# Kernel optimization log

Hardware: AMD Instinct MI355X
Metric: run time of the kernel (lower is better)

## Reference

```python
import jax, jax.numpy as jnp
import numpy as np

B = 2048        # batch of plans
N_LEAF = 1024   # scan nodes (leaves of complete binary tree)
F = 32          # node feature dim
H = 128         # neural-unit hidden dim
O = 32          # unit output dim = 1 (latency) + data_vec_dim (31)


def _mlp_params(key, in_dim, scale=0.05):
    k1, k2, k3 = jax.random.split(key, 3)
    return (
        jax.random.normal(k1, (in_dim, H), jnp.float32) * scale, jnp.zeros((H,), jnp.float32),
        jax.random.normal(k2, (H, H), jnp.float32) * scale, jnp.zeros((H,), jnp.float32),
        jax.random.normal(k3, (H, O), jnp.float32) * scale, jnp.zeros((O,), jnp.float32),
    )


def setup_inputs() -> dict:
    key = jax.random.key(0)
    k1, k2, k3, k4 = jax.random.split(key, 4)
    leaf_feats = jax.random.normal(k1, (B, N_LEAF, F), jnp.float32)
    # internal nodes stored level-by-level bottom-up: 512, 256, ..., 1  (total 1023)
    internal_feats = jax.random.normal(k2, (B, N_LEAF - 1, F), jnp.float32)
    sW1, sb1, sW2, sb2, sW3, sb3 = _mlp_params(k3, F)           # Scan unit (0 children)
    jW1, jb1, jW2, jb2, jW3, jb3 = _mlp_params(k4, F + 2 * O)   # Join unit (2 children)
    return dict(leaf_feats=leaf_feats, internal_feats=internal_feats,
                sW1=sW1, sb1=sb1, sW2=sW2, sb2=sb2, sW3=sW3, sb3=sb3,
                jW1=jW1, jb1=jb1, jW2=jW2, jb2=jb2, jW3=jW3, jb3=jb3)


def _unit(x, W1, b1, W2, b2, W3, b3):
    # Neural unit: 2 hidden ReLU layers -> O outputs (latency + data vector)
    h = jax.nn.relu(x @ W1 + b1)
    h = jax.nn.relu(h @ W2 + b2)
    return h @ W3 + b3


def reference(leaf_feats, internal_feats,
              sW1, sb1, sW2, sb2, sW3, sb3,
              jW1, jb1, jW2, jb2, jW3, jb3):
    # Leaves: Scan unit on node features alone
    cur = _unit(leaf_feats, sW1, sb1, sW2, sb2, sW3, sb3)  # [B, 1024, O]
    off, n = 0, N_LEAF // 2
    while n >= 1:  # static loop over tree levels (bottom-up)
        feats = internal_feats[:, off:off + n]             # [B, n, F]
        children = cur.reshape(B, n, 2 * O)                # concat of 2 child outputs
        x = jnp.concatenate([feats, children], axis=-1)    # [B, n, F + 2O]
        cur = _unit(x, jW1, jb1, jW2, jb2, jW3, jb3)       # [B, n, O]
        off += n
        n //= 2
    return cur[:, 0, 0]  # root latency (output[:, 0]) per plan -> [B]
```

## Files before the change

kernel.cpp:

```cpp
#include <hip/hip_runtime.h>
#include <hip/hip_bf16.h>


typedef _Float16 f16;
typedef _Float16 f16x8 __attribute__((ext_vector_type(8)));
typedef _Float16 f16x4 __attribute__((ext_vector_type(4)));
typedef float    f32x4 __attribute__((ext_vector_type(4)));

#define MFMA16(a, b, c) __builtin_amdgcn_mfma_f32_16x16x32_f16((a), (b), (c), 0, 0, 0)

#define OFF_S1 0
#define OFF_S2 4096
#define OFF_S3 20480
#define OFF_J1 24576
#define OFF_J2 36864
#define OFF_J3 53248
#define W_TOTAL 57344
#define CURA_BYTE_OFF 114688

__global__ void prep_weights(const float* __restrict__ sW1,
                             const float* __restrict__ sW2,
                             const float* __restrict__ sW3,
                             const float* __restrict__ jW1,
                             const float* __restrict__ jW2,
                             const float* __restrict__ jW3,
                             f16* __restrict__ wbuf)
{
    int idx = blockIdx.x * 256 + threadIdx.x;
    if (idx >= W_TOTAL) return;
    const float* W;
    int off, M, K;
    if (idx < OFF_S2)      { off = OFF_S1; M = 128; K = 32;  W = sW1; }
    else if (idx < OFF_S3) { off = OFF_S2; M = 128; K = 128; W = sW2; }
    else if (idx < OFF_J1) { off = OFF_S3; M = 32;  K = 128; W = sW3; }
    else if (idx < OFF_J2) { off = OFF_J1; M = 128; K = 96;  W = jW1; }
    else if (idx < OFF_J3) { off = OFF_J2; M = 128; K = 128; W = jW2; }
    else                   { off = OFF_J3; M = 32;  K = 128; W = jW3; }
    int r = idx - off;
    int m = r / K;
    int k = r - m * K;
    wbuf[idx] = (f16)W[(size_t)k * M + m];
}

__device__ __forceinline__ void gload16(const void* g, void* l)
{
    __builtin_amdgcn_global_load_lds(
        (const __attribute__((address_space(1))) void*)g,
        (__attribute__((address_space(3))) void*)l,
        16, 0, 0);
}

template <bool LEAF>
__global__ __launch_bounds__(256, 3)
void mlp_level(const float* __restrict__ feats,
               const f16*   __restrict__ cur_in,
               f16*         __restrict__ cur_out,
               float*       __restrict__ out_final,
               const f16*   __restrict__ W1t,
               const f16*   __restrict__ W2t,
               const f16*   __restrict__ W3t,
               const float* __restrict__ b1,
               const float* __restrict__ b2,
               const float* __restrict__ b3,
               int rows, int log2n, int foff, int is_last)
{
    constexpr int K1    = LEAF ? 32 : 96;
    constexpr int NK1   = LEAF ? 1 : 3;
    constexpr int PITCH = 136;

    __shared__ __align__(16) f16   h1[32 * PITCH];
    __shared__ __align__(16) f16   h2[32 * PITCH];
    __shared__ __align__(16) float fstage[2][32 * 32];
    __shared__ __align__(16) f16   cstage[(LEAF ? 1 : 2)][32 * 64];

    const int tid  = threadIdx.x;
    const int wave = tid >> 6;
    const int lane = tid & 63;
    const int n    = lane & 15;
    const int q    = lane >> 4;
    const int n7   = n & 7;
    const int mrow = 32 * wave;
    const int l3g  = wave & 1;
    const int l3h  = wave >> 1;

    const int srow   = (wave << 3) + (lane >> 3);
    const int schunk = (lane & 7) ^ (lane >> 3);

    f16x8 A1[2][NK1], A2[2][4], A3[4];
#pragma unroll
    for (int mt = 0; mt < 2; ++mt)
#pragma unroll
        for (int ks = 0; ks < NK1; ++ks)
            A1[mt][ks] = *(const f16x8*)(W1t + (size_t)(mrow + 16 * mt + n) * K1 + 32 * ks + 8 * q);
#pragma unroll
    for (int mt = 0; mt < 2; ++mt)
#pragma unroll
        for (int ks = 0; ks < 4; ++ks)
            A2[mt][ks] = *(const f16x8*)(W2t + (size_t)(mrow + 16 * mt + n) * 128 + 32 * ks + 8 * q);
#pragma unroll
    for (int ks = 0; ks < 4; ++ks)
        A3[ks] = *(const f16x8*)(W3t + (size_t)(16 * l3h + n) * 128 + 32 * ks + 8 * q);

    f32x4 bf1[2], bf2[2], bf3;
#pragma unroll
    for (int mt = 0; mt < 2; ++mt) {
        bf1[mt] = *(const f32x4*)(b1 + mrow + 16 * mt + 4 * q);
        bf2[mt] = *(const f32x4*)(b2 + mrow + 16 * mt + 4 * q);
    }
    bf3 = *(const f32x4*)(b3 + 16 * l3h + 4 * q);

    auto stage = [&](int tg0, int sb) {
        int gr = tg0 + srow;
        const float* fsrc;
        if constexpr (LEAF) {
            fsrc = feats + (size_t)gr * 32 + schunk * 4;
        } else {
            int bb = gr >> log2n;
            int ii = gr & ((1 << log2n) - 1);
            fsrc = feats + ((size_t)bb * 1023 + foff + ii) * 32 + schunk * 4;
        }
        gload16(fsrc, &fstage[sb][wave * 256]);
        if constexpr (!LEAF)
            gload16(cur_in + (size_t)gr * 64 + schunk * 8, &cstage[sb][wave * 512]);
    };

    const int stride = gridDim.x * 32;
    int g0 = blockIdx.x * 32;
    if (g0 >= rows) return;

    int rb = 0;
    stage(g0, 0);

    for (; g0 < rows; g0 += stride) {
        int gnext = g0 + stride;
        stage(gnext < rows ? gnext : g0, rb ^ 1);

        if constexpr (LEAF) asm volatile("s_waitcnt vmcnt(1)" ::: "memory");
        else                asm volatile("s_waitcnt vmcnt(2)" ::: "memory");
        __builtin_amdgcn_s_barrier();

        f32x4 C[2][2];
#pragma unroll
        for (int g = 0; g < 2; ++g)
#pragma unroll
            for (int mt = 0; mt < 2; ++mt) C[g][mt] = bf1[mt];

#pragma unroll
        for (int g = 0; g < 2; ++g) {
            const int r = 16 * g + n;
            f32x4 fa = *(const f32x4*)(&fstage[rb][r * 32 + (((2 * q)     ^ n7) * 4)]);
            f32x4 fb = *(const f32x4*)(&fstage[rb][r * 32 + (((2 * q + 1) ^ n7) * 4)]);
            f16x8 Bf;
#pragma unroll
            for (int j = 0; j < 4; ++j) {
                Bf[j]     = (f16)fa[j];
                Bf[4 + j] = (f16)fb[j];
            }
#pragma unroll
            for (int mt = 0; mt < 2; ++mt) C[g][mt] = MFMA16(A1[mt][0], Bf, C[g][mt]);
            if constexpr (!LEAF) {
                f16x8 cl = *(const f16x8*)(&cstage[rb][r * 64 + ((q       ^ n7) * 8)]);
                f16x8 cr = *(const f16x8*)(&cstage[rb][r * 64 + (((4 + q) ^ n7) * 8)]);
#pragma unroll
                for (int mt = 0; mt < 2; ++mt) C[g][mt] = MFMA16(A1[mt][1], cl, C[g][mt]);
#pragma unroll
                for (int mt = 0; mt < 2; ++mt) C[g][mt] = MFMA16(A1[mt][2], cr, C[g][mt]);
            }
        }
#pragma unroll
        for (int g = 0; g < 2; ++g)
#pragma unroll
            for (int mt = 0; mt < 2; ++mt) {
                f16x4 pk;
                pk[0] = (f16)fmaxf(C[g][mt][0], 0.0f);
                pk[1] = (f16)fmaxf(C[g][mt][1], 0.0f);
                pk[2] = (f16)fmaxf(C[g][mt][2], 0.0f);
                pk[3] = (f16)fmaxf(C[g][mt][3], 0.0f);
                *(f16x4*)(h1 + (16 * g + n) * PITCH + mrow + 16 * mt + 4 * q) = pk;
            }
        asm volatile("s_waitcnt lgkmcnt(0)" ::: "memory");
        __builtin_amdgcn_s_barrier();

#pragma unroll
        for (int g = 0; g < 2; ++g)
#pragma unroll
            for (int mt = 0; mt < 2; ++mt) C[g][mt] = bf2[mt];
#pragma unroll
        for (int ks = 0; ks < 4; ++ks)
#pragma unroll
            for (int g = 0; g < 2; ++g) {
                f16x8 Bf = *(const f16x8*)(h1 + (16 * g + n) * PITCH + 32 * ks + 8 * q);
#pragma unroll
                for (int mt = 0; mt < 2; ++mt) C[g][mt] = MFMA16(A2[mt][ks], Bf, C[g][mt]);
            }
#pragma unroll
        for (int g = 0; g < 2; ++g)
#pragma unroll
            for (int mt = 0; mt < 2; ++mt) {
                f16x4 pk;
                pk[0] = (f16)fmaxf(C[g][mt][0], 0.0f);
                pk[1] = (f16)fmaxf(C[g][mt][1], 0.0f);
                pk[2] = (f16)fmaxf(C[g][mt][2], 0.0f);
                pk[3] = (f16)fmaxf(C[g][mt][3], 0.0f);
                *(f16x4*)(h2 + (16 * g + n) * PITCH + mrow + 16 * mt + 4 * q) = pk;
            }
        asm volatile("s_waitcnt lgkmcnt(0)" ::: "memory");
        __builtin_amdgcn_s_barrier();

        f32x4 C3 = bf3;
#pragma unroll
        for (int ks = 0; ks < 4; ++ks) {
            f16x8 Bf = *(const f16x8*)(h2 + (16 * l3g + n) * PITCH + 32 * ks + 8 * q);
            C3 = MFMA16(A3[ks], Bf, C3);
        }

        if (is_last) {
            if (l3h == 0 && q == 0) out_final[g0 + 16 * l3g + n] = C3[0];
        } else {
            f16x4 pk;
            pk[0] = (f16)C3[0]; pk[1] = (f16)C3[1]; pk[2] = (f16)C3[2]; pk[3] = (f16)C3[3];
            *(f16x4*)(cur_out + (size_t)(g0 + 16 * l3g + n) * 32 + 16 * l3h + 4 * q) = pk;
        }

        rb ^= 1;
    }
}

extern "C" void kernel_launch(void* const* d_in, const int* in_sizes, int n_in,
                              void* d_out, int out_size, void* d_ws, size_t ws_size,
                              hipStream_t stream)
{
    const float* leaf_feats     = (const float*)d_in[0];
    const float* internal_feats = (const float*)d_in[1];
    const float* sW1 = (const float*)d_in[2];  const float* sb1 = (const float*)d_in[3];
    const float* sW2 = (const float*)d_in[4];  const float* sb2 = (const float*)d_in[5];
    const float* sW3 = (const float*)d_in[6];  const float* sb3 = (const float*)d_in[7];
    const float* jW1 = (const float*)d_in[8];  const float* jb1 = (const float*)d_in[9];
    const float* jW2 = (const float*)d_in[10]; const float* jb2 = (const float*)d_in[11];
    const float* jW3 = (const float*)d_in[12]; const float* jb3 = (const float*)d_in[13];

    f16* wbuf = (f16*)d_ws;
    f16* curA = (f16*)((char*)d_ws + CURA_BYTE_OFF);
    f16* curB = (f16*)((char*)d_ws + CURA_BYTE_OFF + 134217728);

    prep_weights<<<(W_TOTAL + 255) / 256, 256, 0, stream>>>(
        sW1, sW2, sW3, jW1, jW2, jW3, wbuf);

    mlp_level<true><<<2048, 256, 0, stream>>>(
        leaf_feats, nullptr, curA, nullptr,
        wbuf + OFF_S1, wbuf + OFF_S2, wbuf + OFF_S3,
        sb1, sb2, sb3,
        2048 * 1024, 0, 0, 0);

    const f16* cin = curA;
    f16* cout = curB;
    int off = 0, lg = 9;
    for (int nlev = 512; nlev >= 1; nlev >>= 1, --lg) {
        int rows  = 2048 * nlev;
        int iters = rows / 32;
        int grid  = iters < 2048 ? iters : 2048;
        mlp_level<false><<<grid, 256, 0, stream>>>(
            internal_feats, cin, cout, (float*)d_out,
            wbuf + OFF_J1, wbuf + OFF_J2, wbuf + OFF_J3,
            jb1, jb2, jb3,
            rows, lg, off, (nlev == 1) ? 1 : 0);
        off += nlev;
        f16* t = cout; cout = (f16*)cin; cin = t;
    }
}
```

Baseline: 787.5 us.

## Software-pipeline the three MLP layers across tiles with one barrier per stage

```diff
diff --git a/kernel.cpp b/kernel.cpp
--- a/kernel.cpp
+++ b/kernel.cpp
@@ -8,6 +8,10 @@
 typedef float    f32x4 __attribute__((ext_vector_type(4)));
 
 #define MFMA16(a, b, c) __builtin_amdgcn_mfma_f32_16x16x32_f16((a), (b), (c), 0, 0, 0)
+
+#define VMCNT(N) asm volatile("s_waitcnt vmcnt(" #N ")" ::: "memory")
+#define LGKM0    asm volatile("s_waitcnt lgkmcnt(0)" ::: "memory")
+#define BARRIER() do { __builtin_amdgcn_s_barrier(); __builtin_amdgcn_sched_barrier(0); } while (0)
 
 #define OFF_S1 0
 #define OFF_S2 4096
@@ -50,7 +54,7 @@
         16, 0, 0);
 }
 
-template <bool LEAF>
+template <bool LEAF, bool LAST>
 __global__ __launch_bounds__(256, 3)
 void mlp_level(const float* __restrict__ feats,
                const f16*   __restrict__ cur_in,
@@ -62,16 +66,16 @@
                const float* __restrict__ b1,
                const float* __restrict__ b2,
                const float* __restrict__ b3,
-               int rows, int log2n, int foff, int is_last)
+               int log2n, int foff, int nt)
 {
-    constexpr int K1    = LEAF ? 32 : 96;
-    constexpr int NK1   = LEAF ? 1 : 3;
-    constexpr int PITCH = 136;
-
-    __shared__ __align__(16) f16   h1[32 * PITCH];
-    __shared__ __align__(16) f16   h2[32 * PITCH];
-    __shared__ __align__(16) float fstage[2][32 * 32];
+    constexpr int K1  = LEAF ? 32 : 96;
+    constexpr int NK1 = LEAF ? 1 : 3;
+
+    __shared__ __align__(16) f16   h1[2][32 * 128];
+    __shared__ __align__(16) f16   h2[2][32 * 128];
+    __shared__ __align__(16) float fstage[3][32 * 32];
     __shared__ __align__(16) f16   cstage[(LEAF ? 1 : 2)][32 * 64];
+    __shared__ __align__(16) float bias_lds[288];
 
     const int tid  = threadIdx.x;
     const int wave = tid >> 6;
@@ -86,6 +90,10 @@
     const int srow   = (wave << 3) + (lane >> 3);
     const int schunk = (lane & 7) ^ (lane >> 3);
 
+    if (tid < 128) bias_lds[tid] = b1[tid];
+    else           bias_lds[tid] = b2[tid - 128];
+    if (tid < 32)  bias_lds[256 + tid] = b3[tid];
+
     f16x8 A1[2][NK1], A2[2][4], A3[4];
 #pragma unroll
     for (int mt = 0; mt < 2; ++mt)
@@ -101,15 +109,10 @@
     for (int ks = 0; ks < 4; ++ks)
         A3[ks] = *(const f16x8*)(W3t + (size_t)(16 * l3h + n) * 128 + 32 * ks + 8 * q);
 
-    f32x4 bf1[2], bf2[2], bf3;
-#pragma unroll
-    for (int mt = 0; mt < 2; ++mt) {
-        bf1[mt] = *(const f32x4*)(b1 + mrow + 16 * mt + 4 * q);
-        bf2[mt] = *(const f32x4*)(b2 + mrow + 16 * mt + 4 * q);
-    }
-    bf3 = *(const f32x4*)(b3 + 16 * l3h + 4 * q);
-
-    auto stage = [&](int tg0, int sb) {
+    const int stride = gridDim.x * 32;
+    const int base   = blockIdx.x * 32;
+
+    auto stage_f = [&](int tg0, int sb) {
         int gr = tg0 + srow;
         const float* fsrc;
         if constexpr (LEAF) {
@@ -120,47 +123,35 @@
             fsrc = feats + ((size_t)bb * 1023 + foff + ii) * 32 + schunk * 4;
         }
         gload16(fsrc, &fstage[sb][wave * 256]);
-        if constexpr (!LEAF)
-            gload16(cur_in + (size_t)gr * 64 + schunk * 8, &cstage[sb][wave * 512]);
-    };
-
-    const int stride = gridDim.x * 32;
-    int g0 = blockIdx.x * 32;
-    if (g0 >= rows) return;
-
-    int rb = 0;
-    stage(g0, 0);
-
-    for (; g0 < rows; g0 += stride) {
-        int gnext = g0 + stride;
-        stage(gnext < rows ? gnext : g0, rb ^ 1);
-
-        if constexpr (LEAF) asm volatile("s_waitcnt vmcnt(1)" ::: "memory");
-        else                asm volatile("s_waitcnt vmcnt(2)" ::: "memory");
-        __builtin_amdgcn_s_barrier();
-
+    };
+    auto stage_c = [&](int tg0, int sb) {
+        int gr = tg0 + srow;
+        gload16(cur_in + (size_t)gr * 64 + schunk * 8, &cstage[sb][wave * 512]);
+    };
+
+    auto doL1 = [&](int t, int g0) {
+        const int fb = t % 3;
+        const int hb = t & 1;
         f32x4 C[2][2];
 #pragma unroll
-        for (int g = 0; g < 2; ++g)
-#pragma unroll
-            for (int mt = 0; mt < 2; ++mt) C[g][mt] = bf1[mt];
-
+        for (int mt = 0; mt < 2; ++mt) {
+            f32x4 bv = *(const f32x4*)&bias_lds[mrow + 16 * mt + 4 * q];
+            C[0][mt] = bv; C[1][mt] = bv;
+        }
 #pragma unroll
         for (int g = 0; g < 2; ++g) {
             const int r = 16 * g + n;
-            f32x4 fa = *(const f32x4*)(&fstage[rb][r * 32 + (((2 * q)     ^ n7) * 4)]);
-            f32x4 fb = *(const f32x4*)(&fstage[rb][r * 32 + (((2 * q + 1) ^ n7) * 4)]);
+            f32x4 fa = *(const f32x4*)&fstage[fb][r * 32 + (((2 * q)     ^ n7) << 2)];
+            f32x4 fv = *(const f32x4*)&fstage[fb][r * 32 + (((2 * q + 1) ^ n7) << 2)];
             f16x8 Bf;
 #pragma unroll
-            for (int j = 0; j < 4; ++j) {
-                Bf[j]     = (f16)fa[j];
-                Bf[4 + j] = (f16)fb[j];
-            }
+            for (int j = 0; j < 4; ++j) { Bf[j] = (f16)fa[j]; Bf[4 + j] = (f16)fv[j]; }
 #pragma unroll
             for (int mt = 0; mt < 2; ++mt) C[g][mt] = MFMA16(A1[mt][0], Bf, C[g][mt]);
             if constexpr (!LEAF) {
-                f16x8 cl = *(const f16x8*)(&cstage[rb][r * 64 + ((q       ^ n7) * 8)]);
-                f16x8 cr = *(const f16x8*)(&cstage[rb][r * 64 + (((4 + q) ^ n7) * 8)]);
+                const int cb = t & 1;
+                f16x8 cl = *(const f16x8*)&cstage[cb][r * 64 + (( q      ^ n7) << 3)];
+                f16x8 cr = *(const f16x8*)&cstage[cb][r * 64 + (((4 + q) ^ n7) << 3)];
 #pragma unroll
                 for (int mt = 0; mt < 2; ++mt) C[g][mt] = MFMA16(A1[mt][1], cl, C[g][mt]);
 #pragma unroll
@@ -176,20 +167,24 @@
                 pk[1] = (f16)fmaxf(C[g][mt][1], 0.0f);
                 pk[2] = (f16)fmaxf(C[g][mt][2], 0.0f);
                 pk[3] = (f16)fmaxf(C[g][mt][3], 0.0f);
-                *(f16x4*)(h1 + (16 * g + n) * PITCH + mrow + 16 * mt + 4 * q) = pk;
+                const int ch = 4 * wave + 2 * mt + (q >> 1);
+                *(f16x4*)&h1[hb][(16 * g + n) * 128 + ((ch ^ n7) << 3) + 4 * (q & 1)] = pk;
             }
-        asm volatile("s_waitcnt lgkmcnt(0)" ::: "memory");
-        __builtin_amdgcn_s_barrier();
-
-#pragma unroll
-        for (int g = 0; g < 2; ++g)
-#pragma unroll
-            for (int mt = 0; mt < 2; ++mt) C[g][mt] = bf2[mt];
+    };
+
+    auto doL2 = [&](int t) {
+        const int hb = t & 1;
+        f32x4 C[2][2];
+#pragma unroll
+        for (int mt = 0; mt < 2; ++mt) {
+            f32x4 bv = *(const f32x4*)&bias_lds[128 + mrow + 16 * mt + 4 * q];
+            C[0][mt] = bv; C[1][mt] = bv;
+        }
 #pragma unroll
         for (int ks = 0; ks < 4; ++ks)
 #pragma unroll
             for (int g = 0; g < 2; ++g) {
-                f16x8 Bf = *(const f16x8*)(h1 + (16 * g + n) * PITCH + 32 * ks + 8 * q);
+                f16x8 Bf = *(const f16x8*)&h1[hb][(16 * g + n) * 128 + (((4 * ks + q) ^ n7) << 3)];
 #pragma unroll
                 for (int mt = 0; mt < 2; ++mt) C[g][mt] = MFMA16(A2[mt][ks], Bf, C[g][mt]);
             }
@@ -202,27 +197,87 @@
                 pk[1] = (f16)fmaxf(C[g][mt][1], 0.0f);
                 pk[2] = (f16)fmaxf(C[g][mt][2], 0.0f);
                 pk[3] = (f16)fmaxf(C[g][mt][3], 0.0f);
-                *(f16x4*)(h2 + (16 * g + n) * PITCH + mrow + 16 * mt + 4 * q) = pk;
+                const int ch = 4 * wave + 2 * mt + (q >> 1);
+                *(f16x4*)&h2[hb][(16 * g + n) * 128 + ((ch ^ n7) << 3) + 4 * (q & 1)] = pk;
             }
-        asm volatile("s_waitcnt lgkmcnt(0)" ::: "memory");
-        __builtin_amdgcn_s_barrier();
-
-        f32x4 C3 = bf3;
+    };
+
+    auto doL3 = [&](int t, int g0) {
+        const int hb = t & 1;
+        f32x4 C3 = *(const f32x4*)&bias_lds[256 + 16 * l3h + 4 * q];
 #pragma unroll
         for (int ks = 0; ks < 4; ++ks) {
-            f16x8 Bf = *(const f16x8*)(h2 + (16 * l3g + n) * PITCH + 32 * ks + 8 * q);
+            f16x8 Bf = *(const f16x8*)&h2[hb][(16 * l3g + n) * 128 + (((4 * ks + q) ^ n7) << 3)];
             C3 = MFMA16(A3[ks], Bf, C3);
         }
-
-        if (is_last) {
+        if constexpr (LAST) {
             if (l3h == 0 && q == 0) out_final[g0 + 16 * l3g + n] = C3[0];
         } else {
             f16x4 pk;
             pk[0] = (f16)C3[0]; pk[1] = (f16)C3[1]; pk[2] = (f16)C3[2]; pk[3] = (f16)C3[3];
             *(f16x4*)(cur_out + (size_t)(g0 + 16 * l3g + n) * 32 + 16 * l3h + 4 * q) = pk;
         }
-
-        rb ^= 1;
+    };
+
+    stage_f(base, 0);
+    if (nt > 1) stage_f(base + stride, 1);
+    if constexpr (!LEAF) stage_c(base, 0);
+    LGKM0;
+
+    if (nt >= 6) {
+        if constexpr (LEAF) { VMCNT(1); } else { VMCNT(0); }
+        BARRIER();
+        if constexpr (!LEAF) stage_c(base + stride, 1);
+        stage_f(base + 2 * stride, 2);
+        doL1(0, base);
+        LGKM0;
+        VMCNT(1); BARRIER();
+        if constexpr (!LEAF) stage_c(base + 2 * stride, 0);
+        stage_f(base + 3 * stride, 0);
+        doL1(1, base + stride); doL2(0);
+        LGKM0;
+        VMCNT(1); BARRIER();
+        if constexpr (!LEAF) stage_c(base + 3 * stride, 1);
+        stage_f(base + 4 * stride, 1);
+        doL1(2, base + 2 * stride); doL2(1); doL3(0, base);
+        LGKM0;
+        VMCNT(2); BARRIER();
+        if constexpr (!LEAF) stage_c(base + 4 * stride, 0);
+        stage_f(base + 5 * stride, 2);
+        doL1(3, base + 3 * stride); doL2(2); doL3(1, base + stride);
+        LGKM0;
+        for (int p = 4; p <= nt - 2; ++p) {
+            if constexpr (LEAF) { VMCNT(3); } else { VMCNT(2); }
+            BARRIER();
+            if constexpr (!LEAF) stage_c(base + (p + 1) * stride, (p + 1) & 1);
+            if (p + 2 < nt) stage_f(base + (p + 2) * stride, (p + 2) % 3);
+            doL1(p, base + p * stride);
+            doL2(p - 1);
+            doL3(p - 2, base + (p - 2) * stride);
+            LGKM0;
+        }
+        if constexpr (LEAF) { VMCNT(2); } else { VMCNT(1); }
+        BARRIER();
+        doL1(nt - 1, base + (nt - 1) * stride);
+        doL2(nt - 2);
+        doL3(nt - 3, base + (nt - 3) * stride);
+        LGKM0;
+        BARRIER();
+        doL2(nt - 1);
+        doL3(nt - 2, base + (nt - 2) * stride);
+        LGKM0;
+        BARRIER();
+        doL3(nt - 1, base + (nt - 1) * stride);
+    } else {
+        for (int p = 0; p <= nt + 1; ++p) {
+            VMCNT(0); BARRIER();
+            if constexpr (!LEAF) { if (p + 1 < nt) stage_c(base + (p + 1) * stride, (p + 1) & 1); }
+            if (p + 2 < nt) stage_f(base + (p + 2) * stride, (p + 2) % 3);
+            if (p < nt)              doL1(p, base + p * stride);
+            if (p >= 1 && p <= nt)   doL2(p - 1);
+            if (p >= 2)              doL3(p - 2, base + (p - 2) * stride);
+            LGKM0;
+        }
     }
 }
 
@@ -246,11 +301,11 @@
     prep_weights<<<(W_TOTAL + 255) / 256, 256, 0, stream>>>(
         sW1, sW2, sW3, jW1, jW2, jW3, wbuf);
 
-    mlp_level<true><<<2048, 256, 0, stream>>>(
+    mlp_level<true, false><<<2048, 256, 0, stream>>>(
         leaf_feats, nullptr, curA, nullptr,
         wbuf + OFF_S1, wbuf + OFF_S2, wbuf + OFF_S3,
         sb1, sb2, sb3,
-        2048 * 1024, 0, 0, 0);
+        0, 0, 32);
 
     const f16* cin = curA;
     f16* cout = curB;
@@ -259,11 +314,20 @@
         int rows  = 2048 * nlev;
         int iters = rows / 32;
         int grid  = iters < 2048 ? iters : 2048;
-        mlp_level<false><<<grid, 256, 0, stream>>>(
-            internal_feats, cin, cout, (float*)d_out,
-            wbuf + OFF_J1, wbuf + OFF_J2, wbuf + OFF_J3,
-            jb1, jb2, jb3,
-            rows, lg, off, (nlev == 1) ? 1 : 0);
+        int nt    = iters / grid;
+        if (nlev == 1) {
+            mlp_level<false, true><<<grid, 256, 0, stream>>>(
+                internal_feats, cin, cout, (float*)d_out,
+                wbuf + OFF_J1, wbuf + OFF_J2, wbuf + OFF_J3,
+                jb1, jb2, jb3,
+                lg, off, nt);
+        } else {
+            mlp_level<false, false><<<grid, 256, 0, stream>>>(
+                internal_feats, cin, cout, (float*)d_out,
+                wbuf + OFF_J1, wbuf + OFF_J2, wbuf + OFF_J3,
+                jb1, jb2, jb3,
+                lg, off, nt);
+        }
         off += nlev;
         f16* t = cout; cout = (f16*)cin; cin = t;
     }
```

Result: slower. 856.4 us (+8.7%).

## Software-pipeline MLP levels with register prefetch and fuse top tree levels into one tail kernel

Applied to the files above, without the earlier changes.

```diff
diff --git a/kernel.cpp b/kernel.cpp
--- a/kernel.cpp
+++ b/kernel.cpp
@@ -1,5 +1,4 @@
 #include <hip/hip_runtime.h>
-#include <hip/hip_bf16.h>
 
 
 typedef _Float16 f16;
@@ -8,6 +7,8 @@
 typedef float    f32x4 __attribute__((ext_vector_type(4)));
 
 #define MFMA16(a, b, c) __builtin_amdgcn_mfma_f32_16x16x32_f16((a), (b), (c), 0, 0, 0)
+#define LGKM0    asm volatile("s_waitcnt lgkmcnt(0)" ::: "memory")
+#define BARRIER() do { __builtin_amdgcn_s_barrier(); __builtin_amdgcn_sched_barrier(0); } while (0)
 
 #define OFF_S1 0
 #define OFF_S2 4096
@@ -42,36 +43,25 @@
     wbuf[idx] = (f16)W[(size_t)k * M + m];
 }
 
-__device__ __forceinline__ void gload16(const void* g, void* l)
-{
-    __builtin_amdgcn_global_load_lds(
-        (const __attribute__((address_space(1))) void*)g,
-        (__attribute__((address_space(3))) void*)l,
-        16, 0, 0);
-}
-
 template <bool LEAF>
-__global__ __launch_bounds__(256, 3)
+__global__ __launch_bounds__(256, LEAF ? 4 : 3)
 void mlp_level(const float* __restrict__ feats,
                const f16*   __restrict__ cur_in,
                f16*         __restrict__ cur_out,
-               float*       __restrict__ out_final,
                const f16*   __restrict__ W1t,
                const f16*   __restrict__ W2t,
                const f16*   __restrict__ W3t,
                const float* __restrict__ b1,
                const float* __restrict__ b2,
                const float* __restrict__ b3,
-               int rows, int log2n, int foff, int is_last)
+               int log2n, int foff, int nt)
 {
-    constexpr int K1    = LEAF ? 32 : 96;
-    constexpr int NK1   = LEAF ? 1 : 3;
-    constexpr int PITCH = 136;
-
-    __shared__ __align__(16) f16   h1[32 * PITCH];
-    __shared__ __align__(16) f16   h2[32 * PITCH];
-    __shared__ __align__(16) float fstage[2][32 * 32];
-    __shared__ __align__(16) f16   cstage[(LEAF ? 1 : 2)][32 * 64];
+    constexpr int K1  = LEAF ? 32 : 96;
+    constexpr int NK1 = LEAF ? 1 : 3;
+
+    __shared__ __align__(16) f16   h1[32 * 128];
+    __shared__ __align__(16) f16   h2[2][32 * 128];
+    __shared__ __align__(16) float bias_lds[288];
 
     const int tid  = threadIdx.x;
     const int wave = tid >> 6;
@@ -83,8 +73,9 @@
     const int l3g  = wave & 1;
     const int l3h  = wave >> 1;
 
-    const int srow   = (wave << 3) + (lane >> 3);
-    const int schunk = (lane & 7) ^ (lane >> 3);
+    if (tid < 128) bias_lds[tid] = b1[tid];
+    else           bias_lds[tid] = b2[tid - 128];
+    if (tid < 32)  bias_lds[256 + tid] = b3[tid];
 
     f16x8 A1[2][NK1], A2[2][4], A3[4];
 #pragma unroll
@@ -101,70 +92,49 @@
     for (int ks = 0; ks < 4; ++ks)
         A3[ks] = *(const f16x8*)(W3t + (size_t)(16 * l3h + n) * 128 + 32 * ks + 8 * q);
 
-    f32x4 bf1[2], bf2[2], bf3;
-#pragma unroll
-    for (int mt = 0; mt < 2; ++mt) {
-        bf1[mt] = *(const f32x4*)(b1 + mrow + 16 * mt + 4 * q);
-        bf2[mt] = *(const f32x4*)(b2 + mrow + 16 * mt + 4 * q);
-    }
-    bf3 = *(const f32x4*)(b3 + 16 * l3h + 4 * q);
-
-    auto stage = [&](int tg0, int sb) {
-        int gr = tg0 + srow;
-        const float* fsrc;
-        if constexpr (LEAF) {
-            fsrc = feats + (size_t)gr * 32 + schunk * 4;
-        } else {
-            int bb = gr >> log2n;
-            int ii = gr & ((1 << log2n) - 1);
-            fsrc = feats + ((size_t)bb * 1023 + foff + ii) * 32 + schunk * 4;
-        }
-        gload16(fsrc, &fstage[sb][wave * 256]);
-        if constexpr (!LEAF)
-            gload16(cur_in + (size_t)gr * 64 + schunk * 8, &cstage[sb][wave * 512]);
+    LGKM0; BARRIER();
+
+    struct PF { f32x4 fa[2], fb[2]; f16x8 cl[2], cr[2]; };
+    auto load_pf = [&](int g0, PF& p) {
+#pragma unroll
+        for (int g = 0; g < 2; ++g) {
+            int gr = g0 + 16 * g + n;
+            const float* frow;
+            if constexpr (LEAF) {
+                frow = feats + (size_t)gr * 32;
+            } else {
+                int bb = gr >> log2n;
+                int ii = gr & ((1 << log2n) - 1);
+                frow = feats + ((size_t)bb * 1023 + foff + ii) * 32;
+            }
+            p.fa[g] = *(const f32x4*)(frow + 8 * q);
+            p.fb[g] = *(const f32x4*)(frow + 8 * q + 4);
+            if constexpr (!LEAF) {
+                p.cl[g] = *(const f16x8*)(cur_in + (size_t)(2 * gr) * 32 + 8 * q);
+                p.cr[g] = *(const f16x8*)(cur_in + (size_t)(2 * gr) * 32 + 32 + 8 * q);
+            }
+        }
     };
 
-    const int stride = gridDim.x * 32;
-    int g0 = blockIdx.x * 32;
-    if (g0 >= rows) return;
-
-    int rb = 0;
-    stage(g0, 0);
-
-    for (; g0 < rows; g0 += stride) {
-        int gnext = g0 + stride;
-        stage(gnext < rows ? gnext : g0, rb ^ 1);
-
-        if constexpr (LEAF) asm volatile("s_waitcnt vmcnt(1)" ::: "memory");
-        else                asm volatile("s_waitcnt vmcnt(2)" ::: "memory");
-        __builtin_amdgcn_s_barrier();
-
+    auto doL1 = [&](const PF& p) {
         f32x4 C[2][2];
 #pragma unroll
-        for (int g = 0; g < 2; ++g)
-#pragma unroll
-            for (int mt = 0; mt < 2; ++mt) C[g][mt] = bf1[mt];
-
+        for (int mt = 0; mt < 2; ++mt) {
+            f32x4 bv = *(const f32x4*)&bias_lds[mrow + 16 * mt + 4 * q];
+            C[0][mt] = bv; C[1][mt] = bv;
+        }
 #pragma unroll
         for (int g = 0; g < 2; ++g) {
-            const int r = 16 * g + n;
-            f32x4 fa = *(const f32x4*)(&fstage[rb][r * 32 + (((2 * q)     ^ n7) * 4)]);
-            f32x4 fb = *(const f32x4*)(&fstage[rb][r * 32 + (((2 * q + 1) ^ n7) * 4)]);
             f16x8 Bf;
 #pragma unroll
-            for (int j = 0; j < 4; ++j) {
-                Bf[j]     = (f16)fa[j];
-                Bf[4 + j] = (f16)fb[j];
-            }
+            for (int j = 0; j < 4; ++j) { Bf[j] = (f16)p.fa[g][j]; Bf[4 + j] = (f16)p.fb[g][j]; }
 #pragma unroll
             for (int mt = 0; mt < 2; ++mt) C[g][mt] = MFMA16(A1[mt][0], Bf, C[g][mt]);
             if constexpr (!LEAF) {
-                f16x8 cl = *(const f16x8*)(&cstage[rb][r * 64 + ((q       ^ n7) * 8)]);
-                f16x8 cr = *(const f16x8*)(&cstage[rb][r * 64 + (((4 + q) ^ n7) * 8)]);
-#pragma unroll
-                for (int mt = 0; mt < 2; ++mt) C[g][mt] = MFMA16(A1[mt][1], cl, C[g][mt]);
-#pragma unroll
-                for (int mt = 0; mt < 2; ++mt) C[g][mt] = MFMA16(A1[mt][2], cr, C[g][mt]);
+#pragma unroll
+                for (int mt = 0; mt < 2; ++mt) C[g][mt] = MFMA16(A1[mt][1], p.cl[g], C[g][mt]);
+#pragma unroll
+                for (int mt = 0; mt < 2; ++mt) C[g][mt] = MFMA16(A1[mt][2], p.cr[g], C[g][mt]);
             }
         }
 #pragma unroll
@@ -176,23 +146,29 @@
                 pk[1] = (f16)fmaxf(C[g][mt][1], 0.0f);
                 pk[2] = (f16)fmaxf(C[g][mt][2], 0.0f);
                 pk[3] = (f16)fmaxf(C[g][mt][3], 0.0f);
-                *(f16x4*)(h1 + (16 * g + n) * PITCH + mrow + 16 * mt + 4 * q) = pk;
-            }
-        asm volatile("s_waitcnt lgkmcnt(0)" ::: "memory");
-        __builtin_amdgcn_s_barrier();
-
-#pragma unroll
-        for (int g = 0; g < 2; ++g)
-#pragma unroll
-            for (int mt = 0; mt < 2; ++mt) C[g][mt] = bf2[mt];
+                const int ch = 4 * wave + 2 * mt + (q >> 1);
+                *(f16x4*)&h1[(16 * g + n) * 128 + ((ch ^ n7) << 3) + 4 * (q & 1)] = pk;
+            }
+    };
+
+    auto doL2 = [&](int t) {
+        const int hb = t & 1;
+        f32x4 C[2][2];
+#pragma unroll
+        for (int mt = 0; mt < 2; ++mt) {
+            f32x4 bv = *(const f32x4*)&bias_lds[128 + mrow + 16 * mt + 4 * q];
+            C[0][mt] = bv; C[1][mt] = bv;
+        }
+        __builtin_amdgcn_s_setprio(1);
 #pragma unroll
         for (int ks = 0; ks < 4; ++ks)
 #pragma unroll
             for (int g = 0; g < 2; ++g) {
-                f16x8 Bf = *(const f16x8*)(h1 + (16 * g + n) * PITCH + 32 * ks + 8 * q);
+                f16x8 Bf = *(const f16x8*)&h1[(16 * g + n) * 128 + (((4 * ks + q) ^ n7) << 3)];
 #pragma unroll
                 for (int mt = 0; mt < 2; ++mt) C[g][mt] = MFMA16(A2[mt][ks], Bf, C[g][mt]);
             }
+        __builtin_amdgcn_s_setprio(0);
 #pragma unroll
         for (int g = 0; g < 2; ++g)
 #pragma unroll
@@ -202,27 +178,199 @@
                 pk[1] = (f16)fmaxf(C[g][mt][1], 0.0f);
                 pk[2] = (f16)fmaxf(C[g][mt][2], 0.0f);
                 pk[3] = (f16)fmaxf(C[g][mt][3], 0.0f);
-                *(f16x4*)(h2 + (16 * g + n) * PITCH + mrow + 16 * mt + 4 * q) = pk;
-            }
-        asm volatile("s_waitcnt lgkmcnt(0)" ::: "memory");
-        __builtin_amdgcn_s_barrier();
-
-        f32x4 C3 = bf3;
+                const int ch = 4 * wave + 2 * mt + (q >> 1);
+                *(f16x4*)&h2[hb][(16 * g + n) * 128 + ((ch ^ n7) << 3) + 4 * (q & 1)] = pk;
+            }
+    };
+
+    auto doL3 = [&](int t, int g0) {
+        const int hb = t & 1;
+        f32x4 C3 = *(const f32x4*)&bias_lds[256 + 16 * l3h + 4 * q];
 #pragma unroll
         for (int ks = 0; ks < 4; ++ks) {
-            f16x8 Bf = *(const f16x8*)(h2 + (16 * l3g + n) * PITCH + 32 * ks + 8 * q);
+            f16x8 Bf = *(const f16x8*)&h2[hb][(16 * l3g + n) * 128 + (((4 * ks + q) ^ n7) << 3)];
             C3 = MFMA16(A3[ks], Bf, C3);
         }
-
-        if (is_last) {
-            if (l3h == 0 && q == 0) out_final[g0 + 16 * l3g + n] = C3[0];
-        } else {
-            f16x4 pk;
-            pk[0] = (f16)C3[0]; pk[1] = (f16)C3[1]; pk[2] = (f16)C3[2]; pk[3] = (f16)C3[3];
-            *(f16x4*)(cur_out + (size_t)(g0 + 16 * l3g + n) * 32 + 16 * l3h + 4 * q) = pk;
-        }
-
-        rb ^= 1;
+        f16x4 pk;
+        pk[0] = (f16)C3[0]; pk[1] = (f16)C3[1]; pk[2] = (f16)C3[2]; pk[3] = (f16)C3[3];
+        *(f16x4*)(cur_out + (size_t)(g0 + 16 * l3g + n) * 32 + 16 * l3h + 4 * q) = pk;
+    };
+
+    const int stride = gridDim.x * 32;
+    const int base   = blockIdx.x * 32;
+
+    PF p;
+    load_pf(base, p);
+    for (int t = 0; t < nt; ++t) {
+        const int g0 = base + t * stride;
+        PF pn;
+        if (t + 1 < nt) load_pf(g0 + stride, pn);
+        doL1(p);
+        if (t > 0) doL3(t - 1, g0 - stride);
+        LGKM0; BARRIER();
+        doL2(t);
+        LGKM0; BARRIER();
+        if (t + 1 < nt) p = pn;
+    }
+    doL3(nt - 1, base + (nt - 1) * stride);
+}
+
+__global__ __launch_bounds__(256, 2)
+void mlp_tail(const float* __restrict__ feats,
+              const f16*   __restrict__ cur_in,
+              float*       __restrict__ out_final,
+              const f16*   __restrict__ W1t,
+              const f16*   __restrict__ W2t,
+              const f16*   __restrict__ W3t,
+              const float* __restrict__ b1,
+              const float* __restrict__ b2,
+              const float* __restrict__ b3)
+{
+    __shared__ __align__(16) f16   h1[32 * 128];
+    __shared__ __align__(16) f16   h2[32 * 128];
+    __shared__ __align__(16) f16   cur_lds[32 * 32];
+    __shared__ __align__(16) float bias_lds[288];
+
+    const int tid  = threadIdx.x;
+    const int wave = tid >> 6;
+    const int lane = tid & 63;
+    const int n    = lane & 15;
+    const int q    = lane >> 4;
+    const int n7   = n & 7;
+    const int mrow = 32 * wave;
+    const int l3g  = wave & 1;
+    const int l3h  = wave >> 1;
+    const int b0   = blockIdx.x * 2;
+
+    if (tid < 128) bias_lds[tid] = b1[tid];
+    else           bias_lds[tid] = b2[tid - 128];
+    if (tid < 32)  bias_lds[256 + tid] = b3[tid];
+
+    f16x8 A1[2][3], A2[2][4], A3[4];
+#pragma unroll
+    for (int mt = 0; mt < 2; ++mt)
+#pragma unroll
+        for (int ks = 0; ks < 3; ++ks)
+            A1[mt][ks] = *(const f16x8*)(W1t + (size_t)(mrow + 16 * mt + n) * 96 + 32 * ks + 8 * q);
+#pragma unroll
+    for (int mt = 0; mt < 2; ++mt)
+#pragma unroll
+        for (int ks = 0; ks < 4; ++ks)
+            A2[mt][ks] = *(const f16x8*)(W2t + (size_t)(mrow + 16 * mt + n) * 128 + 32 * ks + 8 * q);
+#pragma unroll
+    for (int ks = 0; ks < 4; ++ks)
+        A3[ks] = *(const f16x8*)(W3t + (size_t)(16 * l3h + n) * 128 + 32 * ks + 8 * q);
+
+    LGKM0; BARRIER();
+
+    int nlev = 16, lg = 4, fo = 992;
+    for (int lev = 0; lev < 5; ++lev) {
+        const int rows_t = 2 * nlev;
+        f32x4 fa[2], fb[2];
+        f16x8 cl[2], cr[2];
+#pragma unroll
+        for (int g = 0; g < 2; ++g) {
+            int r   = 16 * g + n;
+            int sel = (r >> lg) & 1;
+            int i   = r & (nlev - 1);
+            int rc  = sel * nlev + i;
+            const float* frow = feats + ((size_t)(b0 + sel) * 1023 + fo + i) * 32;
+            fa[g] = *(const f32x4*)(frow + 8 * q);
+            fb[g] = *(const f32x4*)(frow + 8 * q + 4);
+            if (lev == 0) {
+                int gr = (b0 + sel) * 16 + i;
+                cl[g] = *(const f16x8*)(cur_in + (size_t)(2 * gr) * 32 + 8 * q);
+                cr[g] = *(const f16x8*)(cur_in + (size_t)(2 * gr) * 32 + 32 + 8 * q);
+            } else {
+                cl[g] = *(const f16x8*)&cur_lds[(2 * rc) * 32 + 8 * q];
+                cr[g] = *(const f16x8*)&cur_lds[(2 * rc) * 32 + 32 + 8 * q];
+            }
+        }
+        {
+            f32x4 C[2][2];
+#pragma unroll
+            for (int mt = 0; mt < 2; ++mt) {
+                f32x4 bv = *(const f32x4*)&bias_lds[mrow + 16 * mt + 4 * q];
+                C[0][mt] = bv; C[1][mt] = bv;
+            }
+#pragma unroll
+            for (int g = 0; g < 2; ++g) {
+                f16x8 Bf;
+#pragma unroll
+                for (int j = 0; j < 4; ++j) { Bf[j] = (f16)fa[g][j]; Bf[4 + j] = (f16)fb[g][j]; }
+#pragma unroll
+                for (int mt = 0; mt < 2; ++mt) C[g][mt] = MFMA16(A1[mt][0], Bf, C[g][mt]);
+#pragma unroll
+                for (int mt = 0; mt < 2; ++mt) C[g][mt] = MFMA16(A1[mt][1], cl[g], C[g][mt]);
+#pragma unroll
+                for (int mt = 0; mt < 2; ++mt) C[g][mt] = MFMA16(A1[mt][2], cr[g], C[g][mt]);
+            }
+#pragma unroll
+            for (int g = 0; g < 2; ++g)
+#pragma unroll
+                for (int mt = 0; mt < 2; ++mt) {
+                    f16x4 pk;
+                    pk[0] = (f16)fmaxf(C[g][mt][0], 0.0f);
+                    pk[1] = (f16)fmaxf(C[g][mt][1], 0.0f);
+                    pk[2] = (f16)fmaxf(C[g][mt][2], 0.0f);
+                    pk[3] = (f16)fmaxf(C[g][mt][3], 0.0f);
+                    const int ch = 4 * wave + 2 * mt + (q >> 1);
+                    *(f16x4*)&h1[(16 * g + n) * 128 + ((ch ^ n7) << 3) + 4 * (q & 1)] = pk;
+                }
+        }
+        LGKM0; BARRIER();
+        {
+            f32x4 C[2][2];
+#pragma unroll
+            for (int mt = 0; mt < 2; ++mt) {
+                f32x4 bv = *(const f32x4*)&bias_lds[128 + mrow + 16 * mt + 4 * q];
+                C[0][mt] = bv; C[1][mt] = bv;
+            }
+#pragma unroll
+            for (int ks = 0; ks < 4; ++ks)
+#pragma unroll
+                for (int g = 0; g < 2; ++g) {
+                    f16x8 Bf = *(const f16x8*)&h1[(16 * g + n) * 128 + (((4 * ks + q) ^ n7) << 3)];
+#pragma unroll
+                    for (int mt = 0; mt < 2; ++mt) C[g][mt] = MFMA16(A2[mt][ks], Bf, C[g][mt]);
+                }
+#pragma unroll
+            for (int g = 0; g < 2; ++g)
+#pragma unroll
+                for (int mt = 0; mt < 2; ++mt) {
+                    f16x4 pk;
+                    pk[0] = (f16)fmaxf(C[g][mt][0], 0.0f);
+                    pk[1] = (f16)fmaxf(C[g][mt][1], 0.0f);
+                    pk[2] = (f16)fmaxf(C[g][mt][2], 0.0f);
+                    pk[3] = (f16)fmaxf(C[g][mt][3], 0.0f);
+                    const int ch = 4 * wave + 2 * mt + (q >> 1);
+                    *(f16x4*)&h2[(16 * g + n) * 128 + ((ch ^ n7) << 3) + 4 * (q & 1)] = pk;
+                }
+        }
+        LGKM0; BARRIER();
+        {
+            f32x4 C3 = *(const f32x4*)&bias_lds[256 + 16 * l3h + 4 * q];
+#pragma unroll
+            for (int ks = 0; ks < 4; ++ks) {
+                f16x8 Bf = *(const f16x8*)&h2[(16 * l3g + n) * 128 + (((4 * ks + q) ^ n7) << 3)];
+                C3 = MFMA16(A3[ks], Bf, C3);
+            }
+            if (nlev > 1) {
+                int row = 16 * l3g + n;
+                if (row < rows_t) {
+                    f16x4 pk;
+                    pk[0] = (f16)C3[0]; pk[1] = (f16)C3[1]; pk[2] = (f16)C3[2]; pk[3] = (f16)C3[3];
+                    *(f16x4*)&cur_lds[row * 32 + 16 * l3h + 4 * q] = pk;
+                }
+            } else {
+                if (l3g == 0 && l3h == 0 && q == 0 && n < 2)
+                    out_final[b0 + n] = C3[0];
+            }
+        }
+        LGKM0; BARRIER();
+        fo += nlev;
+        nlev >>= 1;
+        --lg;
     }
 }
 
@@ -247,24 +395,30 @@
         sW1, sW2, sW3, jW1, jW2, jW3, wbuf);
 
     mlp_level<true><<<2048, 256, 0, stream>>>(
-        leaf_feats, nullptr, curA, nullptr,
+        leaf_feats, nullptr, curA,
         wbuf + OFF_S1, wbuf + OFF_S2, wbuf + OFF_S3,
         sb1, sb2, sb3,
-        2048 * 1024, 0, 0, 0);
+        0, 0, 32);
 
     const f16* cin = curA;
     f16* cout = curB;
     int off = 0, lg = 9;
-    for (int nlev = 512; nlev >= 1; nlev >>= 1, --lg) {
+    for (int nlev = 512; nlev >= 32; nlev >>= 1, --lg) {
         int rows  = 2048 * nlev;
-        int iters = rows / 32;
-        int grid  = iters < 2048 ? iters : 2048;
+        int tiles = rows / 32;
+        int grid  = tiles < 2048 ? tiles : 2048;
+        int nt    = tiles / grid;
         mlp_level<false><<<grid, 256, 0, stream>>>(
-            internal_feats, cin, cout, (float*)d_out,
+            internal_feats, cin, cout,
             wbuf + OFF_J1, wbuf + OFF_J2, wbuf + OFF_J3,
             jb1, jb2, jb3,
-            rows, lg, off, (nlev == 1) ? 1 : 0);
+            lg, off, nt);
         off += nlev;
         f16* t = cout; cout = (f16*)cin; cin = t;
     }
+
+    mlp_tail<<<1024, 256, 0, stream>>>(
+        internal_feats, cin, (float*)d_out,
+        wbuf + OFF_J1, wbuf + OFF_J2, wbuf + OFF_J3,
+        jb1, jb2, jb3);
 }
```

Result: slower. 1.143 ms (+45.2%).
